# Performance work log

Hardware: AMD Instinct MI355X
Metric: run time of the kernel (lower is better)

## Reference

```python
import jax, jax.numpy as jnp
import numpy as np

V, D, L, H, FF, MAXLEN = 32000, 512, 6, 8, 2048, 4096
B, S = 8, 1024
DH = D // H
EPS = 1e-5


def _pos_encoding(max_len, d_model):
    pos = np.arange(max_len)[:, None].astype(np.float32)
    div = np.exp(np.arange(0, d_model, 2).astype(np.float32) * (-np.log(10000.0) / d_model))
    pe = np.zeros((max_len, d_model), dtype=np.float32)
    pe[:, 0::2] = np.sin(pos * div)
    pe[:, 1::2] = np.cos(pos * div)
    return jnp.asarray(pe)


def setup_inputs() -> dict:
    key = jax.random.key(0)
    ks = jax.random.split(key, 16)
    s = 0.02
    inp = {
        'src': jax.random.randint(ks[0], (B, S), 0, V),
        'mask': jnp.ones((B, 1, 1, S), dtype=jnp.int32),
        'emb': s * jax.random.normal(ks[1], (V, D), dtype=jnp.float32),
        'pe': _pos_encoding(MAXLEN, D),
        # stacked per-layer params [L, ...]; Linear stored as [d_in, d_out]
        'wq': s * jax.random.normal(ks[2], (L, D, D), dtype=jnp.float32),
        'bq': jnp.zeros((L, D), dtype=jnp.float32),
        'wk': s * jax.random.normal(ks[3], (L, D, D), dtype=jnp.float32),
        'bk': jnp.zeros((L, D), dtype=jnp.float32),
        'wv': s * jax.random.normal(ks[4], (L, D, D), dtype=jnp.float32),
        'bv': jnp.zeros((L, D), dtype=jnp.float32),
        'wo': s * jax.random.normal(ks[5], (L, D, D), dtype=jnp.float32),
        'bo': jnp.zeros((L, D), dtype=jnp.float32),
        'w1': s * jax.random.normal(ks[6], (L, D, FF), dtype=jnp.float32),
        'b1': jnp.zeros((L, FF), dtype=jnp.float32),
        'w2': s * jax.random.normal(ks[7], (L, FF, D), dtype=jnp.float32),
        'b2': jnp.zeros((L, D), dtype=jnp.float32),
        'g1': jnp.ones((L, D), dtype=jnp.float32),
        'be1': jnp.zeros((L, D), dtype=jnp.float32),
        'g2': jnp.ones((L, D), dtype=jnp.float32),
        'be2': jnp.zeros((L, D), dtype=jnp.float32),
    }
    return inp


def _layernorm(x, g, b):
    mu = jnp.mean(x, axis=-1, keepdims=True)
    var = jnp.mean(jnp.square(x - mu), axis=-1, keepdims=True)
    return (x - mu) * jax.lax.rsqrt(var + EPS) * g + b


def _encoder(src, mask, emb, pe, wq, bq, wk, bk, wv, bv, wo, bo,
             w1, b1, w2, b2, g1, be1, g2, be2):
    b, s = src.shape
    x = emb[src] + pe[None, :s, :]  # [B,S,D]; dropout is identity (eval)

    def layer(x, p):
        (wq, bq, wk, bk, wv, bv, wo, bo, w1, b1, w2, b2, g1, be1, g2, be2) = p
        def heads(y):
            return y.reshape(b, s, H, DH).transpose(0, 2, 1, 3)  # [B,H,S,Dh]
        Q = heads(x @ wq + bq)
        K = heads(x @ wk + bk)
        Vv = heads(x @ wv + bv)
        scores = jnp.einsum('bhqd,bhkd->bhqk', Q, K) / jnp.sqrt(jnp.float32(DH))
        scores = jnp.where(mask == 0, -jnp.inf, scores)
        attn = jax.nn.softmax(scores, axis=-1)
        out = jnp.einsum('bhqk,bhkd->bhqd', attn, Vv)
        out = out.transpose(0, 2, 1, 3).reshape(b, s, D) @ wo + bo
        x1 = _layernorm(x + out, g1, be1)
        ff = jax.nn.relu(x1 @ w1 + b1) @ w2 + b2
        return _layernorm(x1 + ff, g2, be2), None

    params = (wq, bq, wk, bk, wv, bv, wo, bo, w1, b1, w2, b2, g1, be1, g2, be2)
    x, _ = jax.lax.scan(layer, x, params)
    return x


def reference(src, mask, emb, pe, wq, bq, wk, bk, wv, bv, wo, bo,
              w1, b1, w2, b2, g1, be1, g2, be2):
    return _encoder(src, mask, emb, pe, wq, bq, wk, bk, wv, bv, wo, bo,
                    w1, b1, w2, b2, g1, be1, g2, be2)
```

## Files before the change

### kernel.cpp

```cpp
#include <hip/hip_runtime.h>
#include <stdint.h>

#define DEV static __device__ __forceinline__

typedef float f32x4 __attribute__((ext_vector_type(4)));
typedef short s16x8 __attribute__((ext_vector_type(8)));
typedef unsigned short u16;

constexpr int D   = 512;
constexpr int H   = 8;
constexpr int DHd = 64;
constexpr int S   = 1024;
constexpr int Bn  = 8;
constexpr int L   = 6;
constexpr int FF  = 2048;
constexpr int TOK = Bn * S;
constexpr int QKV = 3 * D;
constexpr int KVB = 64;

DEV u16 f2bf(float f) {
  union { float f; uint32_t u; } v; v.f = f;
  uint32_t u = v.u;
  u += 0x7FFFu + ((u >> 16) & 1u);
  return (u16)(u >> 16);
}

DEV uint32_t cvtpk(float a, float b) {
  uint32_t r;
  asm("v_cvt_pk_bf16_f32 %0, %1, %2" : "=v"(r) : "v"(a), "v"(b));
  return r;
}

DEV float bf2f(u16 u) {
  union { uint32_t u; float f; } t;
  t.u = ((uint32_t)u) << 16;
  return t.f;
}

DEV f32x4 mfma16(s16x8 a, s16x8 b, f32x4 c) {
  return __builtin_amdgcn_mfma_f32_16x16x32_bf16(a, b, c, 0, 0, 0);
}

typedef __attribute__((address_space(1))) const void GV;
typedef __attribute__((address_space(3))) void LV;
DEV void gload_lds16(const u16* g, u16* l) {
  __builtin_amdgcn_global_load_lds((GV*)g, (LV*)l, 16, 0, 0);
}

__global__ __launch_bounds__(256) void wprep4_kernel(const float* __restrict__ wq,
                                                     const float* __restrict__ wk,
                                                     const float* __restrict__ wv,
                                                     const float* __restrict__ wo,
                                                     u16* __restrict__ wqkvT,
                                                     u16* __restrict__ woT) {
  __shared__ float tile[32][33];
  const int z = blockIdx.z, which = z & 3, lyr = z >> 2;
  const float* in = (which == 0 ? wq : which == 1 ? wk : which == 2 ? wv : wo)
                    + (size_t)lyr * D * D;
  u16* out = (which < 3) ? wqkvT + (size_t)lyr * QKV * D + (size_t)which * D * D
                         : woT + (size_t)lyr * D * D;
  const int k0 = blockIdx.x * 32, n0 = blockIdx.y * 32;
  const int tx = (int)threadIdx.x & 31, ty = (int)threadIdx.x >> 5;
#pragma unroll
  for (int i = 0; i < 32; i += 8)
    tile[ty + i][tx] = in[(size_t)(k0 + ty + i) * D + n0 + tx];
  __syncthreads();
#pragma unroll
  for (int i = 0; i < 32; i += 8)
    out[(size_t)(n0 + ty + i) * D + k0 + tx] = f2bf(tile[tx][ty + i]);
}

__global__ __launch_bounds__(256) void wprep_kernel(const float* __restrict__ in,
                                                    u16* __restrict__ out, int K, int N,
                                                    size_t ostride) {
  __shared__ float tile[32][33];
  const int zl = blockIdx.z;
  in  += (size_t)zl * K * N;
  out += (size_t)zl * ostride;
  const int k0 = blockIdx.x * 32, n0 = blockIdx.y * 32;
  const int tx = (int)threadIdx.x & 31, ty = (int)threadIdx.x >> 5;
#pragma unroll
  for (int i = 0; i < 32; i += 8)
    tile[ty + i][tx] = in[(size_t)(k0 + ty + i) * N + n0 + tx];
  __syncthreads();
#pragma unroll
  for (int i = 0; i < 32; i += 8)
    out[(size_t)(n0 + ty + i) * K + k0 + tx] = f2bf(tile[tx][ty + i]);
}

__global__ __launch_bounds__(256) void prep_kernel(const float* __restrict__ bq,
                                                   const float* __restrict__ bk,
                                                   const float* __restrict__ bv,
                                                   const int* __restrict__ mask,
                                                   float* __restrict__ bqkv,
                                                   float* __restrict__ mb,
                                                   int* __restrict__ flags) {
  const int blk = (int)blockIdx.x;
  const int tid = (int)threadIdx.x;
  if (blk < 36) {
    const int i = blk * 256 + tid;
    const int l = i / QKV, r = i % QKV;
    const float* src = (r < D) ? bq : (r < 2 * D ? bk : bv);
    bqkv[i] = src[l * D + (r & (D - 1))];
  } else if (blk < 68) {
    const int i = (blk - 36) * 256 + tid;
    mb[i] = (mask[i] == 0) ? -3e38f : 0.f;
  } else if (tid < 128) {
    const int* m = mask + (tid >> 4) * S + (tid & 15) * 64;
    int all = 1;
#pragma unroll
    for (int j = 0; j < 64; ++j) all &= (m[j] != 0) ? 1 : 0;
    flags[tid] = all;
  }
}

__global__ __launch_bounds__(256) void embed_kernel(const int* __restrict__ src,
                                                    const float* __restrict__ emb,
                                                    const float* __restrict__ pe,
                                                    u16* __restrict__ xb) {
  const int t = (int)blockIdx.x * 4 + ((int)threadIdx.x >> 6);
  const int c = ((int)threadIdx.x & 63) * 8;
  const int s = t & (S - 1);
  const int tok = src[t];
  const float* ep = emb + (size_t)tok * D + c;
  const float* pp = pe + (size_t)s * D + c;
  const f32x4 e0 = *(const f32x4*)ep,       e1 = *(const f32x4*)(ep + 4);
  const f32x4 p0 = *(const f32x4*)pp,       p1 = *(const f32x4*)(pp + 4);
  uint4 ob;
  ob.x = cvtpk(e0[0] + p0[0], e0[1] + p0[1]);
  ob.y = cvtpk(e0[2] + p0[2], e0[3] + p0[3]);
  ob.z = cvtpk(e1[0] + p1[0], e1[1] + p1[1]);
  ob.w = cvtpk(e1[2] + p1[2], e1[3] + p1[3]);
  *(uint4*)(xb + (size_t)t * D + c) = ob;
}

template <int MT, int VMODE, int KSPLIT>
__global__ __launch_bounds__(256) void gemm_kernel(const u16* __restrict__ A,
                                                   const u16* __restrict__ BT,
                                                   const float* __restrict__ bias,
                                                   u16* __restrict__ outB,
                                                   u16* __restrict__ outV,
                                                   int N, int K, int relu) {
  constexpr int BM = MT * 32;
  constexpr float QSCL = 0.125f * 1.44269504089f;
  __shared__ u16 sA[BM * 64];
  __shared__ u16 sB[128 * 64];
  const int tid = (int)threadIdx.x;
  const int w = tid >> 6, l = tid & 63;
  const int wr = w >> 1, wc = w & 1;
  const int lr = l & 15, lg = l >> 4;

  const int nwg = (int)gridDim.x;
  const int bid = (int)blockIdx.x;
  const int wg  = (bid & 7) * (nwg >> 3) + (bid >> 3);
  const int nbn = N >> 7;
  int kidx = 0, rem = wg;
  if constexpr (KSPLIT > 1) {
    const int per = nwg / KSPLIT;
    kidx = wg / per;
    rem  = wg % per;
  }
  const int bm = (rem / nbn) * BM, bn = (rem % nbn) * 128;
  const int KS = K / KSPLIT;

  f32x4 acc[MT][4];
#pragma unroll
  for (int i = 0; i < MT; ++i)
#pragma unroll
    for (int j = 0; j < 4; ++j)
#pragma unroll
      for (int r = 0; r < 4; ++r) acc[i][j][r] = 0.f;

  const int srow = tid >> 3;
  const int sswz = ((tid & 7) ^ (srow & 7)) * 8;
  const int sdst = (tid & 7) * 8;
  const u16* Ag = A + (size_t)(bm + srow) * K + kidx * KS + sswz;
  const u16* Bg = BT + (size_t)(bn + srow) * K + kidx * KS + sswz;
  u16* sAd = sA + srow * 64 + sdst;
  u16* sBd = sB + srow * 64 + sdst;

  for (int kt = 0; kt < KS; kt += 64) {
    __syncthreads();
#pragma unroll
    for (int r = 0; r < BM / 32; ++r)
      gload_lds16(Ag + (size_t)(r * 32) * K + kt, sAd + r * 32 * 64);
#pragma unroll
    for (int r = 0; r < 4; ++r)
      gload_lds16(Bg + (size_t)(r * 32) * K + kt, sBd + r * 32 * 64);
    __syncthreads();
#pragma unroll
    for (int kk = 0; kk < 2; ++kk) {
      s16x8 af[MT], bfr[4];
      const int csw = ((kk * 4 + lg) ^ (lr & 7)) << 3;
#pragma unroll
      for (int mt = 0; mt < MT; ++mt)
        af[mt] = *(const s16x8*)&sA[(wr * MT * 16 + mt * 16 + lr) * 64 + csw];
#pragma unroll
      for (int nt = 0; nt < 4; ++nt)
        bfr[nt] = *(const s16x8*)&sB[(wc * 64 + nt * 16 + lr) * 64 + csw];
#pragma unroll
      for (int mt = 0; mt < MT; ++mt)
#pragma unroll
        for (int nt = 0; nt < 4; ++nt)
          acc[mt][nt] = mfma16(af[mt], bfr[nt], acc[mt][nt]);
    }
  }

#pragma unroll
  for (int mt = 0; mt < MT; ++mt)
#pragma unroll
    for (int nt = 0; nt < 4; ++nt) {
      const int col = bn + wc * 64 + nt * 16 + lr;
      const int row0 = bm + wr * MT * 16 + mt * 16 + lg * 4;
      if constexpr (KSPLIT > 1) {
        u16* op = outB + (size_t)kidx * TOK * N + (size_t)row0 * N + col;
        const uint32_t p01 = cvtpk(acc[mt][nt][0], acc[mt][nt][1]);
        const uint32_t p23 = cvtpk(acc[mt][nt][2], acc[mt][nt][3]);
        op[0]               = (u16)p01;
        op[N]               = (u16)(p01 >> 16);
        op[2 * (size_t)N]   = (u16)p23;
        op[3 * (size_t)N]   = (u16)(p23 >> 16);
      } else {
        const float bv = bias ? bias[col] : 0.f;
        if (VMODE && col >= 2 * D) {
          const int dcol = col - 2 * D;
          const int hh = dcol >> 6, dh = dcol & 63;
          const int bb = row0 >> 10, s = row0 & (S - 1);
          u16* vp = outV + ((size_t)((bb << 3) + hh) * DHd + dh) * S + s;
          *(uint32_t*)(vp)     = cvtpk(acc[mt][nt][0] + bv, acc[mt][nt][1] + bv);
          *(uint32_t*)(vp + 2) = cvtpk(acc[mt][nt][2] + bv, acc[mt][nt][3] + bv);
        } else {
          float v[4];
#pragma unroll
          for (int r = 0; r < 4; ++r) {
            v[r] = acc[mt][nt][r] + bv;
            if (relu) v[r] = fmaxf(v[r], 0.f);
            if (VMODE && col < D) v[r] *= QSCL;
          }
          const size_t o0 = (size_t)row0 * N + col;
          const uint32_t p01 = cvtpk(v[0], v[1]);
          const uint32_t p23 = cvtpk(v[2], v[3]);
          outB[o0]                   = (u16)p01;
          outB[o0 + N]               = (u16)(p01 >> 16);
          outB[o0 + 2 * (size_t)N]   = (u16)p23;
          outB[o0 + 3 * (size_t)N]   = (u16)(p23 >> 16);
        }
      }
    }
}

__global__ __launch_bounds__(512) void attn_kernel(const u16* __restrict__ qkv,
                                                   const u16* __restrict__ vt,
                                                   const int* __restrict__ mflags,
                                                   const float* __restrict__ mb,
                                                   u16* __restrict__ attno) {
  __shared__ u16 sK[2][KVB * 72];
  __shared__ u16 sV[2][KVB * 72];
  __shared__ u16 sP[8][2][16][72];
  const int tid = (int)threadIdx.x;
  const int w = tid >> 6, l = tid & 63;
  const int lr = l & 15, lg = l >> 4;
  const int bid = (int)blockIdx.x;
  const int wg  = (bid & 7) * 32 + (bid >> 3);
  const int bh = wg >> 2, qc = wg & 3;
  const int b = bh >> 3, h = bh & 7;
  const int q0 = qc * 256 + w * 32;

  const u16* qr0 = qkv + (size_t)(b * S + q0 + lr) * QKV + h * DHd;
  const u16* qr1 = qr0 + (size_t)16 * QKV;
  const s16x8 aq0 = *(const s16x8*)(qr0 + lg * 8);
  const s16x8 aq1 = *(const s16x8*)(qr0 + 32 + lg * 8);
  const s16x8 aq2 = *(const s16x8*)(qr1 + lg * 8);
  const s16x8 aq3 = *(const s16x8*)(qr1 + 32 + lg * 8);
  const u16* kbase = qkv + D + (size_t)b * S * QKV + h * DHd;
  const u16* vbase = vt + (size_t)bh * DHd * S;
  const float* mrow0 = mb + b * S;

  s16x8 vones;
#pragma unroll
  for (int i = 0; i < 8; ++i) vones[i] = (short)0x3F80;

  const int srow = tid >> 3;
  const int sc16 = tid & 7;
  const u16* kg = kbase + (size_t)srow * QKV + sc16 * 8;
  const u16* vg = vbase + (size_t)srow * S + sc16 * 8;
  const int soff = srow * 72 + sc16 * 8;

  uint4 ka = *(const uint4*)kg;
  uint4 va = *(const uint4*)vg;
  *(uint4*)&sK[0][soff] = ka;
  *(uint4*)&sV[0][soff] = va;
  ka = *(const uint4*)(kg + (size_t)KVB * QKV);
  va = *(const uint4*)(vg + KVB);
  __syncthreads();

  f32x4 o[2][4], osum[2];
#pragma unroll
  for (int f = 0; f < 2; ++f) {
#pragma unroll
    for (int nt = 0; nt < 4; ++nt)
#pragma unroll
      for (int r = 0; r < 4; ++r) o[f][nt][r] = 0.f;
#pragma unroll
    for (int r = 0; r < 4; ++r) osum[f][r] = 0.f;
  }

  constexpr int NTILE = S / KVB;
  for (int t = 0; t < NTILE; ++t) {
    const int cur = t & 1;
    if (t + 1 < NTILE) {
      *(uint4*)&sK[cur ^ 1][soff] = ka;
      *(uint4*)&sV[cur ^ 1][soff] = va;
    }
    if (t + 2 < NTILE) {
      ka = *(const uint4*)(kg + (size_t)(t + 2) * KVB * QKV);
      va = *(const uint4*)(vg + (t + 2) * KVB);
    }

    f32x4 sa[2][4];
#pragma unroll
    for (int kt = 0; kt < 4; ++kt) {
      const u16* kr = &sK[cur][(kt * 16 + lr) * 72];
      const s16x8 bk0 = *(const s16x8*)(kr + lg * 8);
      const s16x8 bk1 = *(const s16x8*)(kr + 32 + lg * 8);
      f32x4 za, zb;
#pragma unroll
      for (int r = 0; r < 4; ++r) { za[r] = 0.f; zb[r] = 0.f; }
      za = mfma16(bk0, aq0, za);
      sa[0][kt] = mfma16(bk1, aq1, za);
      zb = mfma16(bk0, aq2, zb);
      sa[1][kt] = mfma16(bk1, aq3, zb);
    }

    if (!mflags[(b << 4) + t]) {
#pragma unroll
      for (int kt = 0; kt < 4; ++kt) {
        const f32x4 mk = *(const f32x4*)(mrow0 + t * KVB + kt * 16 + lg * 4);
#pragma unroll
        for (int r = 0; r < 4; ++r) {
          sa[0][kt][r] += mk[r];
          sa[1][kt][r] += mk[r];
        }
      }
    }

#pragma unroll
    for (int f = 0; f < 2; ++f)
#pragma unroll
      for (int kt = 0; kt < 4; ++kt)
#pragma unroll
        for (int r = 0; r < 4; ++r) sa[f][kt][r] = exp2f(sa[f][kt][r]);

#pragma unroll
    for (int f = 0; f < 2; ++f)
#pragma unroll
      for (int kt = 0; kt < 4; ++kt) {
        uint2 pk;
        pk.x = cvtpk(sa[f][kt][0], sa[f][kt][1]);
        pk.y = cvtpk(sa[f][kt][2], sa[f][kt][3]);
        *(uint2*)&sP[w][f][lr][kt * 16 + lg * 4] = pk;
      }

    s16x8 bv[2][4];
#pragma unroll
    for (int ks = 0; ks < 2; ++ks)
#pragma unroll
      for (int nt = 0; nt < 4; ++nt)
        bv[ks][nt] = *(const s16x8*)&sV[cur][(nt * 16 + lr) * 72 + ks * 32 + lg * 8];

#pragma unroll
    for (int ks = 0; ks < 2; ++ks) {
      const s16x8 ap0 = *(const s16x8*)&sP[w][0][lr][ks * 32 + lg * 8];
      const s16x8 ap1 = *(const s16x8*)&sP[w][1][lr][ks * 32 + lg * 8];
      osum[0] = mfma16(ap0, vones, osum[0]);
      osum[1] = mfma16(ap1, vones, osum[1]);
#pragma unroll
      for (int nt = 0; nt < 4; ++nt) {
        o[0][nt] = mfma16(ap0, bv[ks][nt], o[0][nt]);
        o[1][nt] = mfma16(ap1, bv[ks][nt], o[1][nt]);
      }
    }
    __syncthreads();
  }

#pragma unroll
  for (int f = 0; f < 2; ++f) {
    float li[4];
#pragma unroll
    for (int r = 0; r < 4; ++r) li[r] = 1.f / osum[f][r];
#pragma unroll
    for (int nt = 0; nt < 4; ++nt) {
      u16* op = attno + (size_t)(b * S + q0 + f * 16 + lg * 4) * D + h * DHd + nt * 16 + lr;
#pragma unroll
      for (int r = 0; r < 4; r += 2) {
        const uint32_t pk = cvtpk(o[f][nt][r] * li[r], o[f][nt][r + 1] * li[r + 1]);
        op[(size_t)r * D]       = (u16)pk;
        op[(size_t)(r + 1) * D] = (u16)(pk >> 16);
      }
    }
  }
}

template <int NP>
__global__ __launch_bounds__(256) void ln_kernel(const u16* __restrict__ p,
                                                 const float* __restrict__ bias,
                                                 const u16* __restrict__ resid,
                                                 const float* __restrict__ g,
                                                 const float* __restrict__ be,
                                                 float* __restrict__ outf,
                                                 u16* __restrict__ outb) {
  const int w = (int)threadIdx.x >> 6, l = (int)threadIdx.x & 63;
  const int t = (int)blockIdx.x * 4 + w;
  const size_t base = (size_t)t * D + l * 8;
  f32x4 v0 = *(const f32x4*)(bias + l * 8);
  f32x4 v1 = *(const f32x4*)(bias + l * 8 + 4);
  {
    const s16x8 rv = *(const s16x8*)(resid + base);
#pragma unroll
    for (int i = 0; i < 4; ++i) {
      v0[i] += bf2f((u16)rv[i]);
      v1[i] += bf2f((u16)rv[i + 4]);
    }
  }
#pragma unroll
  for (int np = 0; np < NP; ++np) {
    const s16x8 pv = *(const s16x8*)(p + (size_t)np * TOK * D + base);
#pragma unroll
    for (int i = 0; i < 4; ++i) {
      v0[i] += bf2f((u16)pv[i]);
      v1[i] += bf2f((u16)pv[i + 4]);
    }
  }
  float s = 0.f, sq = 0.f;
#pragma unroll
  for (int i = 0; i < 4; ++i) {
    s += v0[i] + v1[i];
    sq += v0[i] * v0[i] + v1[i] * v1[i];
  }
  for (int m = 1; m < 64; m <<= 1) {
    s += __shfl_xor(s, m);
    sq += __shfl_xor(sq, m);
  }
  const float mu = s * (1.0f / D);
  const float var = sq * (1.0f / D) - mu * mu;
  const float rs = rsqrtf(var + 1e-5f);
  const f32x4 g0 = *(const f32x4*)(g + l * 8);
  const f32x4 g1v = *(const f32x4*)(g + l * 8 + 4);
  const f32x4 b0 = *(const f32x4*)(be + l * 8);
  const f32x4 b1v = *(const f32x4*)(be + l * 8 + 4);
  f32x4 y0, y1;
#pragma unroll
  for (int i = 0; i < 4; ++i) {
    y0[i] = (v0[i] - mu) * rs * g0[i] + b0[i];
    y1[i] = (v1[i] - mu) * rs * g1v[i] + b1v[i];
  }
  uint4 ob;
  ob.x = cvtpk(y0[0], y0[1]);
  ob.y = cvtpk(y0[2], y0[3]);
  ob.z = cvtpk(y1[0], y1[1]);
  ob.w = cvtpk(y1[2], y1[3]);
  if (outf) {
    *(f32x4*)(outf + base) = y0;
    *(f32x4*)(outf + base + 4) = y1;
  }
  *(uint4*)(outb + base) = ob;
}

extern "C" void kernel_launch(void* const* d_in, const int* in_sizes, int n_in,
                              void* d_out, int out_size, void* d_ws, size_t ws_size,
                              hipStream_t stream) {
  (void)in_sizes; (void)n_in; (void)out_size; (void)ws_size;
  const int*   src  = (const int*)d_in[0];
  const int*   mask = (const int*)d_in[1];
  const float* emb  = (const float*)d_in[2];
  const float* pe   = (const float*)d_in[3];
  const float* wq = (const float*)d_in[4];  const float* bq = (const float*)d_in[5];
  const float* wk = (const float*)d_in[6];  const float* bk = (const float*)d_in[7];
  const float* wv = (const float*)d_in[8];  const float* bv = (const float*)d_in[9];
  const float* wo = (const float*)d_in[10]; const float* bo = (const float*)d_in[11];
  const float* w1 = (const float*)d_in[12]; const float* b1 = (const float*)d_in[13];
  const float* w2 = (const float*)d_in[14]; const float* b2 = (const float*)d_in[15];
  const float* g1 = (const float*)d_in[16]; const float* be1 = (const float*)d_in[17];
  const float* g2 = (const float*)d_in[18]; const float* be2 = (const float*)d_in[19];

  char* ws = (char*)d_ws;
  size_t off = 0;
  auto alloc = [&](size_t bytes) -> void* {
    void* p = ws + off;
    off += (bytes + 255) & ~(size_t)255;
    return p;
  };

  u16* wqkvT = (u16*)alloc((size_t)L * QKV * D * 2);
  u16* woT   = (u16*)alloc((size_t)L * D * D * 2);
  u16* w1T   = (u16*)alloc((size_t)L * D * FF * 2);
  u16* w2T   = (u16*)alloc((size_t)L * D * FF * 2);
  float* bqkv = (float*)alloc((size_t)L * QKV * 4);
  float* mbf  = (float*)alloc((size_t)TOK * 4);
  int*   mflg = (int*)alloc(128 * 4);
  u16* xb    = (u16*)alloc((size_t)TOK * D * 2);
  u16* x1b   = (u16*)alloc((size_t)TOK * D * 2);
  u16* attno = (u16*)alloc((size_t)TOK * D * 2);
  u16* qkvb  = (u16*)alloc((size_t)TOK * FF * 2);
  u16* vtb   = (u16*)alloc((size_t)TOK * D * 2);
  u16* hbuf  = qkvb;
  u16* pf    = (u16*)alloc((size_t)2 * TOK * D * 2);
  u16* po    = pf;

  const dim3 blk(256);

  wprep4_kernel<<<dim3(16, 16, 4 * L), blk, 0, stream>>>(wq, wk, wv, wo, wqkvT, woT);
  wprep_kernel<<<dim3(16, 64, L), blk, 0, stream>>>(w1, w1T, D, FF, (size_t)D * FF);
  wprep_kernel<<<dim3(64, 16, L), blk, 0, stream>>>(w2, w2T, FF, D, (size_t)D * FF);
  prep_kernel<<<dim3(69), blk, 0, stream>>>(bq, bk, bv, mask, bqkv, mbf, mflg);

  embed_kernel<<<TOK / 4, blk, 0, stream>>>(src, emb, pe, xb);

  for (int lyr = 0; lyr < L; ++lyr) {
    const size_t wOffQ = (size_t)lyr * QKV * D;
    const size_t wOffD = (size_t)lyr * D * D;
    const size_t wOffF = (size_t)lyr * D * FF;
    gemm_kernel<2, 1, 1><<<dim3(128 * 12), blk, 0, stream>>>(xb, wqkvT + wOffQ, bqkv + lyr * QKV,
                                                             qkvb, vtb, QKV, D, 0);
    attn_kernel<<<dim3(256), dim3(512), 0, stream>>>(qkvb, vtb, mflg, mbf, attno);
    gemm_kernel<2, 0, 2><<<dim3(128 * 4 * 2), blk, 0, stream>>>(attno, woT + wOffD, nullptr,
                                                                po, nullptr, D, D, 0);
    ln_kernel<2><<<TOK / 4, blk, 0, stream>>>(po, bo + lyr * D, xb,
                                              g1 + lyr * D, be1 + lyr * D, nullptr, x1b);
    gemm_kernel<2, 0, 1><<<dim3(128 * 16), blk, 0, stream>>>(x1b, w1T + wOffF, b1 + lyr * FF,
                                                             hbuf, nullptr, FF, D, 1);
    gemm_kernel<2, 0, 2><<<dim3(128 * 4 * 2), blk, 0, stream>>>(hbuf, w2T + wOffF, nullptr,
                                                                pf, nullptr, D, FF, 0);
    float* xdst = (lyr == L - 1) ? (float*)d_out : nullptr;
    ln_kernel<2><<<TOK / 4, blk, 0, stream>>>(pf, b2 + lyr * D, x1b,
                                              g2 + lyr * D, be2 + lyr * D, xdst, xb);
  }
}
```

Baseline: 828.1 us.

## Split attention KV range across two wave groups and merge partial sums

New measurement: 860.3 us. 3.9% more time.

```diff
diff --git a/kernel.cpp b/kernel.cpp
--- a/kernel.cpp
+++ b/kernel.cpp
@@ -16,7 +16,6 @@
 constexpr int FF  = 2048;
 constexpr int TOK = Bn * S;
 constexpr int QKV = 3 * D;
-constexpr int KVB = 64;
 
 DEV u16 f2bf(float f) {
   union { float f; uint32_t u; } v; v.f = f;
@@ -249,22 +248,25 @@
     }
 }
 
+constexpr int AKV = 32;
+constexpr int OFF_K = 0;
+constexpr int OFF_V = 9216;
+constexpr int OFF_P = 18432;
 __global__ __launch_bounds__(512) void attn_kernel(const u16* __restrict__ qkv,
                                                    const u16* __restrict__ vt,
                                                    const int* __restrict__ mflags,
                                                    const float* __restrict__ mb,
                                                    u16* __restrict__ attno) {
-  __shared__ u16 sK[2][KVB * 72];
-  __shared__ u16 sV[2][KVB * 72];
-  __shared__ u16 sP[8][2][16][72];
+  __shared__ u16 smem[28672];
   const int tid = (int)threadIdx.x;
   const int w = tid >> 6, l = tid & 63;
   const int lr = l & 15, lg = l >> 4;
+  const int kh = w >> 2;
   const int bid = (int)blockIdx.x;
-  const int wg  = (bid & 7) * 32 + (bid >> 3);
-  const int bh = wg >> 2, qc = wg & 3;
+  const int wg  = (bid & 7) * 64 + (bid >> 3);
+  const int bh = wg >> 3, qc = wg & 7;
   const int b = bh >> 3, h = bh & 7;
-  const int q0 = qc * 256 + w * 32;
+  const int q0 = qc * 128 + (w & 3) * 32;
 
   const u16* qr0 = qkv + (size_t)(b * S + q0 + lr) * QKV + h * DHd;
   const u16* qr1 = qr0 + (size_t)16 * QKV;
@@ -272,26 +274,47 @@
   const s16x8 aq1 = *(const s16x8*)(qr0 + 32 + lg * 8);
   const s16x8 aq2 = *(const s16x8*)(qr1 + lg * 8);
   const s16x8 aq3 = *(const s16x8*)(qr1 + 32 + lg * 8);
-  const u16* kbase = qkv + D + (size_t)b * S * QKV + h * DHd;
-  const u16* vbase = vt + (size_t)bh * DHd * S;
   const float* mrow0 = mb + b * S;
 
   s16x8 vones;
 #pragma unroll
   for (int i = 0; i < 8; ++i) vones[i] = (short)0x3F80;
 
-  const int srow = tid >> 3;
-  const int sc16 = tid & 7;
-  const u16* kg = kbase + (size_t)srow * QKV + sc16 * 8;
-  const u16* vg = vbase + (size_t)srow * S + sc16 * 8;
-  const int soff = srow * 72 + sc16 * 8;
-
-  uint4 ka = *(const uint4*)kg;
-  uint4 va = *(const uint4*)vg;
-  *(uint4*)&sK[0][soff] = ka;
-  *(uint4*)&sV[0][soff] = va;
-  ka = *(const uint4*)(kg + (size_t)KVB * QKV);
-  va = *(const uint4*)(vg + KVB);
+  const int grp  = tid >> 7;
+  const int isV  = grp >> 1;
+  const int skh  = grp & 1;
+  const int t128 = tid & 127;
+  const u16* gp0;
+  const u16* gp1;
+  int lo0, lo1;
+  size_t gstep;
+  if (!isV) {
+    const int r0 = t128 >> 3, c0 = (t128 & 7) * 8;
+    const int r1 = (t128 + 128) >> 3, c1 = ((t128 + 128) & 7) * 8;
+    const u16* kb = qkv + D + (size_t)(b * S + skh * 512) * QKV + h * DHd;
+    gp0 = kb + (size_t)r0 * QKV + c0;
+    gp1 = kb + (size_t)r1 * QKV + c1;
+    lo0 = r0 * 72 + c0;
+    lo1 = r1 * 72 + c1;
+    gstep = (size_t)AKV * QKV;
+  } else {
+    const int r0 = t128 >> 2, c0 = (t128 & 3) * 8;
+    const int r1 = (t128 + 128) >> 2, c1 = ((t128 + 128) & 3) * 8;
+    const u16* vb = vt + (size_t)bh * DHd * S + skh * 512;
+    gp0 = vb + (size_t)r0 * S + c0;
+    gp1 = vb + (size_t)r1 * S + c1;
+    lo0 = r0 * 36 + c0;
+    lo1 = r1 * 36 + c1;
+    gstep = AKV;
+  }
+  const int obase = (isV ? OFF_V : OFF_K) + skh * 2 * 2304;
+
+  uint4 ra = *(const uint4*)gp0;
+  uint4 rb = *(const uint4*)gp1;
+  *(uint4*)&smem[obase + lo0] = ra;
+  *(uint4*)&smem[obase + lo1] = rb;
+  ra = *(const uint4*)(gp0 + gstep);
+  rb = *(const uint4*)(gp1 + gstep);
   __syncthreads();
 
   f32x4 o[2][4], osum[2];
@@ -305,22 +328,26 @@
     for (int r = 0; r < 4; ++r) osum[f][r] = 0.f;
   }
 
-  constexpr int NTILE = S / KVB;
-  for (int t = 0; t < NTILE; ++t) {
+  const int kbK = OFF_K + kh * 2 * 2304;
+  const int kbV = OFF_V + kh * 2 * 2304;
+  const int pbase = OFF_P + (w * 2) * 16 * 40;
+
+  constexpr int NT = 512 / AKV;
+  for (int t = 0; t < NT; ++t) {
     const int cur = t & 1;
-    if (t + 1 < NTILE) {
-      *(uint4*)&sK[cur ^ 1][soff] = ka;
-      *(uint4*)&sV[cur ^ 1][soff] = va;
-    }
-    if (t + 2 < NTILE) {
-      ka = *(const uint4*)(kg + (size_t)(t + 2) * KVB * QKV);
-      va = *(const uint4*)(vg + (t + 2) * KVB);
-    }
-
-    f32x4 sa[2][4];
-#pragma unroll
-    for (int kt = 0; kt < 4; ++kt) {
-      const u16* kr = &sK[cur][(kt * 16 + lr) * 72];
+    if (t + 1 < NT) {
+      *(uint4*)&smem[obase + (cur ^ 1) * 2304 + lo0] = ra;
+      *(uint4*)&smem[obase + (cur ^ 1) * 2304 + lo1] = rb;
+    }
+    if (t + 2 < NT) {
+      ra = *(const uint4*)(gp0 + (size_t)(t + 2) * gstep);
+      rb = *(const uint4*)(gp1 + (size_t)(t + 2) * gstep);
+    }
+
+    f32x4 sa[2][2];
+#pragma unroll
+    for (int kt = 0; kt < 2; ++kt) {
+      const u16* kr = &smem[kbK + cur * 2304 + (kt * 16 + lr) * 72];
       const s16x8 bk0 = *(const s16x8*)(kr + lg * 8);
       const s16x8 bk1 = *(const s16x8*)(kr + 32 + lg * 8);
       f32x4 za, zb;
@@ -332,10 +359,11 @@
       sa[1][kt] = mfma16(bk1, aq3, zb);
     }
 
-    if (!mflags[(b << 4) + t]) {
-#pragma unroll
-      for (int kt = 0; kt < 4; ++kt) {
-        const f32x4 mk = *(const f32x4*)(mrow0 + t * KVB + kt * 16 + lg * 4);
+    const int kofs = kh * 512 + t * AKV;
+    if (!mflags[(b << 4) + (kofs >> 6)]) {
+#pragma unroll
+      for (int kt = 0; kt < 2; ++kt) {
+        const f32x4 mk = *(const f32x4*)(mrow0 + kofs + kt * 16 + lg * 4);
 #pragma unroll
         for (int r = 0; r < 4; ++r) {
           sa[0][kt][r] += mk[r];
@@ -347,55 +375,74 @@
 #pragma unroll
     for (int f = 0; f < 2; ++f)
 #pragma unroll
-      for (int kt = 0; kt < 4; ++kt)
+      for (int kt = 0; kt < 2; ++kt) {
 #pragma unroll
         for (int r = 0; r < 4; ++r) sa[f][kt][r] = exp2f(sa[f][kt][r]);
-
-#pragma unroll
-    for (int f = 0; f < 2; ++f)
-#pragma unroll
-      for (int kt = 0; kt < 4; ++kt) {
         uint2 pk;
         pk.x = cvtpk(sa[f][kt][0], sa[f][kt][1]);
         pk.y = cvtpk(sa[f][kt][2], sa[f][kt][3]);
-        *(uint2*)&sP[w][f][lr][kt * 16 + lg * 4] = pk;
+        *(uint2*)&smem[pbase + (f * 16 + lr) * 40 + kt * 16 + lg * 4] = pk;
       }
 
-    s16x8 bv[2][4];
-#pragma unroll
-    for (int ks = 0; ks < 2; ++ks)
+    s16x8 bv[4];
+#pragma unroll
+    for (int nt = 0; nt < 4; ++nt)
+      bv[nt] = *(const s16x8*)&smem[kbV + cur * 2304 + (nt * 16 + lr) * 36 + lg * 8];
+    const s16x8 ap0 = *(const s16x8*)&smem[pbase + lr * 40 + lg * 8];
+    const s16x8 ap1 = *(const s16x8*)&smem[pbase + (16 + lr) * 40 + lg * 8];
+    osum[0] = mfma16(ap0, vones, osum[0]);
+    osum[1] = mfma16(ap1, vones, osum[1]);
+#pragma unroll
+    for (int nt = 0; nt < 4; ++nt) {
+      o[0][nt] = mfma16(ap0, bv[nt], o[0][nt]);
+      o[1][nt] = mfma16(ap1, bv[nt], o[1][nt]);
+    }
+    __syncthreads();
+  }
+
+  float* ms = (float*)smem;
+  if (kh) {
+    const int slot = ((w - 4) * 64 + l) * 40;
+#pragma unroll
+    for (int f = 0; f < 2; ++f)
 #pragma unroll
       for (int nt = 0; nt < 4; ++nt)
-        bv[ks][nt] = *(const s16x8*)&sV[cur][(nt * 16 + lr) * 72 + ks * 32 + lg * 8];
-
-#pragma unroll
-    for (int ks = 0; ks < 2; ++ks) {
-      const s16x8 ap0 = *(const s16x8*)&sP[w][0][lr][ks * 32 + lg * 8];
-      const s16x8 ap1 = *(const s16x8*)&sP[w][1][lr][ks * 32 + lg * 8];
-      osum[0] = mfma16(ap0, vones, osum[0]);
-      osum[1] = mfma16(ap1, vones, osum[1]);
+        *(f32x4*)&ms[slot + (f * 4 + nt) * 4] = o[f][nt];
+    *(f32x4*)&ms[slot + 32] = osum[0];
+    *(f32x4*)&ms[slot + 36] = osum[1];
+  }
+  __syncthreads();
+  if (!kh) {
+    const int slot = (w * 64 + l) * 40;
+#pragma unroll
+    for (int f = 0; f < 2; ++f)
 #pragma unroll
       for (int nt = 0; nt < 4; ++nt) {
-        o[0][nt] = mfma16(ap0, bv[ks][nt], o[0][nt]);
-        o[1][nt] = mfma16(ap1, bv[ks][nt], o[1][nt]);
+        const f32x4 ov = *(const f32x4*)&ms[slot + (f * 4 + nt) * 4];
+#pragma unroll
+        for (int r = 0; r < 4; ++r) o[f][nt][r] += ov[r];
       }
-    }
-    __syncthreads();
-  }
-
-#pragma unroll
-  for (int f = 0; f < 2; ++f) {
-    float li[4];
-#pragma unroll
-    for (int r = 0; r < 4; ++r) li[r] = 1.f / osum[f][r];
-#pragma unroll
-    for (int nt = 0; nt < 4; ++nt) {
-      u16* op = attno + (size_t)(b * S + q0 + f * 16 + lg * 4) * D + h * DHd + nt * 16 + lr;
-#pragma unroll
-      for (int r = 0; r < 4; r += 2) {
-        const uint32_t pk = cvtpk(o[f][nt][r] * li[r], o[f][nt][r + 1] * li[r + 1]);
-        op[(size_t)r * D]       = (u16)pk;
-        op[(size_t)(r + 1) * D] = (u16)(pk >> 16);
+    const f32x4 s0 = *(const f32x4*)&ms[slot + 32];
+    const f32x4 s1 = *(const f32x4*)&ms[slot + 36];
+#pragma unroll
+    for (int r = 0; r < 4; ++r) {
+      osum[0][r] += s0[r];
+      osum[1][r] += s1[r];
+    }
+#pragma unroll
+    for (int f = 0; f < 2; ++f) {
+      float li[4];
+#pragma unroll
+      for (int r = 0; r < 4; ++r) li[r] = 1.f / osum[f][r];
+#pragma unroll
+      for (int nt = 0; nt < 4; ++nt) {
+        u16* op = attno + (size_t)(b * S + q0 + f * 16 + lg * 4) * D + h * DHd + nt * 16 + lr;
+#pragma unroll
+        for (int r = 0; r < 4; r += 2) {
+          const uint32_t pk = cvtpk(o[f][nt][r] * li[r], o[f][nt][r + 1] * li[r + 1]);
+          op[(size_t)r * D]       = (u16)pk;
+          op[(size_t)(r + 1) * D] = (u16)(pk >> 16);
+        }
       }
     }
   }
@@ -522,7 +569,7 @@
     const size_t wOffF = (size_t)lyr * D * FF;
     gemm_kernel<2, 1, 1><<<dim3(128 * 12), blk, 0, stream>>>(xb, wqkvT + wOffQ, bqkv + lyr * QKV,
                                                              qkvb, vtb, QKV, D, 0);
-    attn_kernel<<<dim3(256), dim3(512), 0, stream>>>(qkvb, vtb, mflg, mbf, attno);
+    attn_kernel<<<dim3(512), dim3(512), 0, stream>>>(qkvb, vtb, mflg, mbf, attno);
     gemm_kernel<2, 0, 2><<<dim3(128 * 4 * 2), blk, 0, stream>>>(attno, woT + wOffD, nullptr,
                                                                 po, nullptr, D, D, 0);
     ln_kernel<2><<<TOK / 4, blk, 0, stream>>>(po, bo + lyr * D, xb,
```

## Double-buffer GEMM LDS tiles to overlap global loads with MFMA compute

Applied to the files above, without the earlier changes.

New measurement: 838.3 us. No clear change (+1.2%).

```diff
diff --git a/kernel.cpp b/kernel.cpp
--- a/kernel.cpp
+++ b/kernel.cpp
@@ -141,10 +141,11 @@
                                                    u16* __restrict__ outB,
                                                    u16* __restrict__ outV,
                                                    int N, int K, int relu) {
+  static_assert(MT == 2, "vmcnt count hard-coded for MT=2 (6 loads/thread)");
   constexpr int BM = MT * 32;
   constexpr float QSCL = 0.125f * 1.44269504089f;
-  __shared__ u16 sA[BM * 64];
-  __shared__ u16 sB[128 * 64];
+  __shared__ u16 sA[2 * BM * 64];
+  __shared__ u16 sB[2 * 128 * 64];
   const int tid = (int)threadIdx.x;
   const int w = tid >> 6, l = tid & 63;
   const int wr = w >> 1, wc = w & 1;
@@ -176,35 +177,56 @@
   const int sdst = (tid & 7) * 8;
   const u16* Ag = A + (size_t)(bm + srow) * K + kidx * KS + sswz;
   const u16* Bg = BT + (size_t)(bn + srow) * K + kidx * KS + sswz;
-  u16* sAd = sA + srow * 64 + sdst;
-  u16* sBd = sB + srow * 64 + sdst;
-
-  for (int kt = 0; kt < KS; kt += 64) {
-    __syncthreads();
+
+  auto stage = [&](int kt, int buf) {
+    u16* ad = sA + buf * BM * 64 + srow * 64 + sdst;
+    u16* bd = sB + buf * 128 * 64 + srow * 64 + sdst;
 #pragma unroll
     for (int r = 0; r < BM / 32; ++r)
-      gload_lds16(Ag + (size_t)(r * 32) * K + kt, sAd + r * 32 * 64);
+      gload_lds16(Ag + (size_t)(r * 32) * K + kt, ad + r * 32 * 64);
 #pragma unroll
     for (int r = 0; r < 4; ++r)
-      gload_lds16(Bg + (size_t)(r * 32) * K + kt, sBd + r * 32 * 64);
-    __syncthreads();
+      gload_lds16(Bg + (size_t)(r * 32) * K + kt, bd + r * 32 * 64);
+  };
+  auto compute = [&](int buf) {
+    const u16* a0 = sA + buf * BM * 64;
+    const u16* b0 = sB + buf * 128 * 64;
 #pragma unroll
     for (int kk = 0; kk < 2; ++kk) {
       s16x8 af[MT], bfr[4];
       const int csw = ((kk * 4 + lg) ^ (lr & 7)) << 3;
 #pragma unroll
       for (int mt = 0; mt < MT; ++mt)
-        af[mt] = *(const s16x8*)&sA[(wr * MT * 16 + mt * 16 + lr) * 64 + csw];
+        af[mt] = *(const s16x8*)&a0[(wr * MT * 16 + mt * 16 + lr) * 64 + csw];
 #pragma unroll
       for (int nt = 0; nt < 4; ++nt)
-        bfr[nt] = *(const s16x8*)&sB[(wc * 64 + nt * 16 + lr) * 64 + csw];
+        bfr[nt] = *(const s16x8*)&b0[(wc * 64 + nt * 16 + lr) * 64 + csw];
 #pragma unroll
       for (int mt = 0; mt < MT; ++mt)
 #pragma unroll
         for (int nt = 0; nt < 4; ++nt)
           acc[mt][nt] = mfma16(af[mt], bfr[nt], acc[mt][nt]);
     }
-  }
+  };
+
+  stage(0, 0);
+  const int NT = KS >> 6;
+  int cur = 0;
+  for (int t = 0; t < NT - 1; ++t) {
+    __builtin_amdgcn_s_barrier();
+    stage((t + 1) * 64, cur ^ 1);
+    asm volatile("s_waitcnt vmcnt(6)" ::: "memory");
+    __builtin_amdgcn_sched_barrier(0);
+    __builtin_amdgcn_s_barrier();
+    __builtin_amdgcn_sched_barrier(0);
+    compute(cur);
+    cur ^= 1;
+  }
+  asm volatile("s_waitcnt vmcnt(0)" ::: "memory");
+  __builtin_amdgcn_sched_barrier(0);
+  __builtin_amdgcn_s_barrier();
+  __builtin_amdgcn_sched_barrier(0);
+  compute(cur);
 
 #pragma unroll
   for (int mt = 0; mt < MT; ++mt)
```
